# Kernel tuning notes

Hardware: AMD Instinct MI355X
Metric: run time of the kernel (lower is better)

## Reference

```python
import math
import jax, jax.numpy as jnp
import numpy as np
from jax import lax

# ---- fixed (non-learned) kernels, built exactly as in Canny.__init__ ----
def _sobel_2d(k=5):
    r = np.linspace(-(k // 2), k // 2, k).astype(np.float32)
    x, y = np.meshgrid(r, r, indexing='ij')
    den = x ** 2 + y ** 2
    den[:, k // 2] = 1.0
    return (x / den / 6.0).astype(np.float32)

_S = _sobel_2d(5)
W_SY = jnp.asarray(_S.reshape(1, 1, 5, 5))            # sobel_y weight
W_SX = jnp.asarray(_S.T.reshape(1, 1, 5, 5))          # sobel_x weight (transposed)

_pos = [(0, 1), (2, 1), (1, 0), (1, 2), (0, 0), (2, 2), (0, 2), (2, 0)]
_ksel = np.zeros((8, 1, 3, 3), dtype=np.float32)
for _i, (_a, _b) in enumerate(_pos):
    _ksel[_i, 0, _a, _b] = 1.0
W_SEL = jnp.asarray(_ksel)
SEL_IDS = jnp.asarray(np.array([[0, 1], [4, 5], [2, 3], [6, 7],
                                [0, 1], [4, 5], [2, 3], [6, 7]], dtype=np.int32))
W_HYST = jnp.ones((1, 1, 3, 3), dtype=jnp.float32)

_DN = ('NCHW', 'OIHW', 'NCHW')

def _conv_reflect(x, w, pad):
    x = jnp.pad(x, ((0, 0), (0, 0), (pad, pad), (pad, pad)), mode='reflect')
    return lax.conv_general_dilated(x, w, (1, 1), 'VALID', dimension_numbers=_DN)

def _conv_zero(x, w, pad):
    return lax.conv_general_dilated(x, w, (1, 1), ((pad, pad), (pad, pad)),
                                    dimension_numbers=_DN)

THRESH_LO = 0.1
THRESH_HI = 0.1

def setup_inputs() -> dict:
    key = jax.random.key(0)
    images = jax.random.uniform(key, (16, 3, 512, 512), dtype=jnp.float32)
    return {'images': images}

def reference(images):
    # shift from [-1,1] to [0,1] if needed
    images = jnp.where(images.min() < -0.001, (images + 1.0) * 0.5, images)
    # channel L2 norm -> [B,1,H,W], normalize by global max
    mag = jnp.linalg.norm(images, axis=1, keepdims=True)
    mag = mag / mag.max()
    sobel_x = _conv_reflect(mag, W_SX, 2)
    sobel_y = _conv_reflect(mag, W_SY, 2)
    grad_mag = jnp.sqrt(sobel_x ** 2 + sobel_y ** 2)             # [B,1,H,W]
    phase = jnp.arctan2(sobel_x, sobel_y + 1e-5)
    phase = jnp.mod(jnp.round(phase / (math.pi / 4)) + 4.0, 8.0).astype(jnp.int32)
    selections = _conv_zero(grad_mag, W_SEL, 1)                  # [B,8,H,W]
    neb_ids = SEL_IDS[phase[:, 0]]                               # [B,H,W,2]
    nebs = jnp.take_along_axis(selections, jnp.transpose(neb_ids, (0, 3, 1, 2)), axis=1)
    # phase-dependent non-maximum suppression
    mask = (grad_mag <= nebs[:, 0:1]) | (grad_mag < nebs[:, 1:2])
    grad_mag = jnp.where(mask, 0.0, grad_mag)
    # low threshold
    grad_mag = jnp.where(grad_mag < THRESH_LO, 0.0, grad_mag)
    # hysteresis
    weak_mask = (grad_mag < THRESH_HI) & (grad_mag > THRESH_LO)
    high_mask = grad_mag > THRESH_HI
    high_nebs = _conv_reflect(high_mask.astype(jnp.float32), W_HYST, 1)
    weak_keep = weak_mask & (high_nebs > 0)
    kill = (~weak_keep) & (~high_mask)
    grad_mag = jnp.where(kill, 0.0, grad_mag)
    # String_Finder: binarize edges at 0.1
    b_edges = jnp.where(grad_mag > 0.1, 1.0, 0.0)
    sobel = jnp.concatenate([sobel_y, sobel_x], axis=1)          # [B,2,H,W]
    return b_edges, sobel
```

## Files before the change

### kernel.cpp

```cpp
#include <hip/hip_runtime.h>
#include <math.h>

#define HH 512
#define WW 512
#define HW (HH*WW)

__device__ __constant__ float WS5[25] = {
  -2.0f/8.0f/6.0f, -2.0f/5.0f/6.0f, -2.0f/1.0f/6.0f, -2.0f/5.0f/6.0f, -2.0f/8.0f/6.0f,
  -1.0f/5.0f/6.0f, -1.0f/2.0f/6.0f, -1.0f/1.0f/6.0f, -1.0f/2.0f/6.0f, -1.0f/5.0f/6.0f,
   0.0f,            0.0f,            0.0f,            0.0f,            0.0f,
   1.0f/5.0f/6.0f,  1.0f/2.0f/6.0f,  1.0f/1.0f/6.0f,  1.0f/2.0f/6.0f,  1.0f/5.0f/6.0f,
   2.0f/8.0f/6.0f,  2.0f/5.0f/6.0f,  2.0f/1.0f/6.0f,  2.0f/5.0f/6.0f,  2.0f/8.0f/6.0f
};

__device__ __forceinline__ int refl(int i) {
  if (i < 0) return -i;
  if (i >= HH) return 2*HH - 2 - i;
  return i;
}

__device__ __forceinline__ float sumsq3(float r, float g, float b) {
  return __fadd_rn(__fadd_rn(__fmul_rn(r,r), __fmul_rn(g,g)), __fmul_rn(b,b));
}

__global__ __launch_bounds__(256) void k1_sumsq(const float* __restrict__ img,
                                                float* __restrict__ ss,
                                                float* __restrict__ partials) {
  int gid = blockIdx.x * 256 + threadIdx.x;
  int n  = gid >> 16;
  int p4 = gid & 65535;
  const float* base = img + (size_t)n * 3 * HW;
  float4 r = ((const float4*)(base        ))[p4];
  float4 g = ((const float4*)(base +   HW ))[p4];
  float4 b = ((const float4*)(base + 2*HW ))[p4];
  float4 s;
  s.x = sumsq3(r.x, g.x, b.x);
  s.y = sumsq3(r.y, g.y, b.y);
  s.z = sumsq3(r.z, g.z, b.z);
  s.w = sumsq3(r.w, g.w, b.w);
  ((float4*)ss)[gid] = s;

  float m = fmaxf(fmaxf(s.x, s.y), fmaxf(s.z, s.w));
  #pragma unroll
  for (int off = 32; off > 0; off >>= 1)
    m = fmaxf(m, __shfl_down(m, off));
  __shared__ float sm[4];
  int lane = threadIdx.x & 63, wv = threadIdx.x >> 6;
  if (lane == 0) sm[wv] = m;
  __syncthreads();
  if (threadIdx.x == 0)
    partials[blockIdx.x] = fmaxf(fmaxf(sm[0], sm[1]), fmaxf(sm[2], sm[3]));
}

__global__ __launch_bounds__(256) void k1b_reduce(const float* __restrict__ partials,
                                                  float* __restrict__ ssmax) {
  float m = 0.0f;
  #pragma unroll
  for (int i = 0; i < 16; ++i)
    m = fmaxf(m, partials[threadIdx.x + 256 * i]);
  #pragma unroll
  for (int off = 32; off > 0; off >>= 1)
    m = fmaxf(m, __shfl_down(m, off));
  __shared__ float sm[4];
  int lane = threadIdx.x & 63, wv = threadIdx.x >> 6;
  if (lane == 0) sm[wv] = m;
  __syncthreads();
  if (threadIdx.x == 0)
    ssmax[0] = fmaxf(fmaxf(sm[0], sm[1]), fmaxf(sm[2], sm[3]));
}

__global__ __launch_bounds__(256) void k2_norm(float* __restrict__ ssmag,
                                               const float* __restrict__ ssmax) {
  int gid = blockIdx.x * 256 + threadIdx.x;
  float mm = sqrtf(ssmax[0]);
  float4 s = ((const float4*)ssmag)[gid];
  float4 o;
  o.x = __fdiv_rn(sqrtf(s.x), mm);
  o.y = __fdiv_rn(sqrtf(s.y), mm);
  o.z = __fdiv_rn(sqrtf(s.z), mm);
  o.w = __fdiv_rn(sqrtf(s.w), mm);
  ((float4*)ssmag)[gid] = o;
}

__global__ __launch_bounds__(256) void k3_sobel(const float* __restrict__ mag,
                                                float* __restrict__ sobel_out,
                                                float* __restrict__ gm,
                                                unsigned char* __restrict__ pairb) {
  int x = blockIdx.x * 64 + threadIdx.x;
  int y = blockIdx.y * 4  + threadIdx.y;
  int n = blockIdx.z;
  const float* mp = mag + (size_t)n * HW;
  double asy = 0.0, asx = 0.0;
  #pragma unroll
  for (int a = 0; a < 5; ++a) {
    int ry = refl(y + a - 2);
    const float* row = mp + ry * WW;
    #pragma unroll
    for (int b = 0; b < 5; ++b) {
      int rx = refl(x + b - 2);
      double v = (double)row[rx];
      asy += v * (double)WS5[a*5 + b];
      asx += v * (double)WS5[b*5 + a];
    }
  }
  float fsy = (float)asy, fsx = (float)asx;
  int p = y * WW + x;
  sobel_out[(size_t)n * 2 * HW + p]      = fsy;
  sobel_out[(size_t)n * 2 * HW + HW + p] = fsx;
  float g = sqrtf(__fadd_rn(__fmul_rn(fsx, fsx), __fmul_rn(fsy, fsy)));
  gm[(size_t)n * HW + p] = g;
  float ph = atan2f(fsx, __fadd_rn(fsy, 1e-5f));
  float pf = __fdiv_rn(ph, 0.78539816339744830962f);
  float r  = rintf(pf);
  int ip = ((int)r + 4) & 7;
  pairb[(size_t)n * HW + p] = (unsigned char)(ip & 3);
}

__global__ __launch_bounds__(256) void k4_nms(const float* __restrict__ gm,
                                              const unsigned char* __restrict__ pairb,
                                              float* __restrict__ edges) {
  int x = blockIdx.x * 64 + threadIdx.x;
  int y = blockIdx.y * 4  + threadIdx.y;
  int n = blockIdx.z;
  const float* gp = gm + (size_t)n * HW;
  int p = y * WW + x;
  float g = gp[p];
  int pr = pairb[(size_t)n * HW + p];
  const int dy0[4] = {-1, -1,  0, -1};
  const int dx0[4] = { 0, -1, -1,  1};
  const int dy1[4] = { 1,  1,  0,  1};
  const int dx1[4] = { 0,  1,  1, -1};
  int y0 = y + dy0[pr], x0 = x + dx0[pr];
  int y1 = y + dy1[pr], x1 = x + dx1[pr];
  float n0 = (y0 >= 0 && y0 < HH && x0 >= 0 && x0 < WW) ? gp[y0 * WW + x0] : 0.0f;
  float n1 = (y1 >= 0 && y1 < HH && x1 >= 0 && x1 < WW) ? gp[y1 * WW + x1] : 0.0f;
  bool mask = (g <= n0) || (g < n1);
  edges[(size_t)n * HW + p] = (!mask && (g > 0.1f)) ? 1.0f : 0.0f;
}

extern "C" void kernel_launch(void* const* d_in, const int* in_sizes, int n_in,
                              void* d_out, int out_size, void* d_ws, size_t ws_size,
                              hipStream_t stream) {
  const float* img = (const float*)d_in[0];
  float* out = (float*)d_out;
  char* ws = (char*)d_ws;

  float* ssmax    = (float*)ws;
  float* partials = (float*)(ws + 256);
  float* ssmag    = (float*)(ws + 256 + 16384);
  float* gm       = (float*)(ws + 256 + 16384 + 16777216);
  unsigned char* pairb = (unsigned char*)(ws + 256 + 16384 + 2*16777216);

  float* edges = out;
  float* sobel = out + 4194304;

  k1_sumsq  <<<dim3(4096), dim3(256), 0, stream>>>(img, ssmag, partials);
  k1b_reduce<<<dim3(1),    dim3(256), 0, stream>>>(partials, ssmax);
  k2_norm   <<<dim3(4096), dim3(256), 0, stream>>>(ssmag, ssmax);
  dim3 blk(64, 4, 1), grd(8, 128, 16);
  k3_sobel<<<grd, blk, 0, stream>>>(ssmag, sobel, gm, pairb);
  k4_nms  <<<grd, blk, 0, stream>>>(gm, pairb, edges);
}
```

Before: 149.1 us.

## Fuse normalization into Sobel kernel with shared-memory halo tile

Removes the separate normalization pass by computing sqrt(ss)/max while loading an 8x68 halo tile into shared memory inside the Sobel kernel. The Sobel taps then read from LDS instead of doing 25 reflected global loads per pixel. This drops one full read+write pass over a 16 MB buffer and one launch. In exchange, the sqrt and divide are recomputed for halo elements (8x68 loads per 4x64 outputs, about 2.1x), and a block barrier is added.

Measured after the change: 142.9 us. -4.1%, faster.

```diff
diff --git a/kernel.cpp b/kernel.cpp
--- a/kernel.cpp
+++ b/kernel.cpp
@@ -69,36 +69,37 @@
     ssmax[0] = fmaxf(fmaxf(sm[0], sm[1]), fmaxf(sm[2], sm[3]));
 }
 
-__global__ __launch_bounds__(256) void k2_norm(float* __restrict__ ssmag,
-                                               const float* __restrict__ ssmax) {
-  int gid = blockIdx.x * 256 + threadIdx.x;
-  float mm = sqrtf(ssmax[0]);
-  float4 s = ((const float4*)ssmag)[gid];
-  float4 o;
-  o.x = __fdiv_rn(sqrtf(s.x), mm);
-  o.y = __fdiv_rn(sqrtf(s.y), mm);
-  o.z = __fdiv_rn(sqrtf(s.z), mm);
-  o.w = __fdiv_rn(sqrtf(s.w), mm);
-  ((float4*)ssmag)[gid] = o;
-}
-
-__global__ __launch_bounds__(256) void k3_sobel(const float* __restrict__ mag,
+__global__ __launch_bounds__(256) void k3_sobel(const float* __restrict__ ss,
+                                                const float* __restrict__ ssmax,
                                                 float* __restrict__ sobel_out,
                                                 float* __restrict__ gm,
                                                 unsigned char* __restrict__ pairb) {
-  int x = blockIdx.x * 64 + threadIdx.x;
-  int y = blockIdx.y * 4  + threadIdx.y;
-  int n = blockIdx.z;
-  const float* mp = mag + (size_t)n * HW;
+  __shared__ float magS[8 * 68];
+  int tx = threadIdx.x;
+  int ty = threadIdx.y;
+  int x0 = blockIdx.x * 64;
+  int y0 = blockIdx.y * 4;
+  int n  = blockIdx.z;
+  const float* sp = ss + (size_t)n * HW;
+  float mm = sqrtf(ssmax[0]);
+
+  int tid = ty * 64 + tx;
+  for (int i = tid; i < 8 * 68; i += 256) {
+    int r = i / 68, c = i - r * 68;
+    int gy = refl(y0 - 2 + r);
+    int gx = refl(x0 - 2 + c);
+    magS[i] = __fdiv_rn(sqrtf(sp[gy * WW + gx]), mm);
+  }
+  __syncthreads();
+
+  int x = x0 + tx;
+  int y = y0 + ty;
   double asy = 0.0, asx = 0.0;
   #pragma unroll
   for (int a = 0; a < 5; ++a) {
-    int ry = refl(y + a - 2);
-    const float* row = mp + ry * WW;
     #pragma unroll
     for (int b = 0; b < 5; ++b) {
-      int rx = refl(x + b - 2);
-      double v = (double)row[rx];
+      double v = (double)magS[(ty + a) * 68 + (tx + b)];
       asy += v * (double)WS5[a*5 + b];
       asx += v * (double)WS5[b*5 + a];
     }
@@ -147,17 +148,16 @@
 
   float* ssmax    = (float*)ws;
   float* partials = (float*)(ws + 256);
-  float* ssmag    = (float*)(ws + 256 + 16384);
+  float* ssbuf    = (float*)(ws + 256 + 16384);
   float* gm       = (float*)(ws + 256 + 16384 + 16777216);
   unsigned char* pairb = (unsigned char*)(ws + 256 + 16384 + 2*16777216);
 
   float* edges = out;
   float* sobel = out + 4194304;
 
-  k1_sumsq  <<<dim3(4096), dim3(256), 0, stream>>>(img, ssmag, partials);
+  k1_sumsq  <<<dim3(4096), dim3(256), 0, stream>>>(img, ssbuf, partials);
   k1b_reduce<<<dim3(1),    dim3(256), 0, stream>>>(partials, ssmax);
-  k2_norm   <<<dim3(4096), dim3(256), 0, stream>>>(ssmag, ssmax);
   dim3 blk(64, 4, 1), grd(8, 128, 16);
-  k3_sobel<<<grd, blk, 0, stream>>>(ssmag, sobel, gm, pairb);
+  k3_sobel<<<grd, blk, 0, stream>>>(ssbuf, ssmax, sobel, gm, pairb);
   k4_nms  <<<grd, blk, 0, stream>>>(gm, pairb, edges);
 }
```
